# Kernel optimization log

Measured on AMD Instinct MI355X. Metric: run time of the kernel, lower is better.

The kernel has to match this reference:

```python
import jax, jax.numpy as jnp
import numpy as np
import math

L, D, H = 4, 256, 8
HD = D // H
B, SQ, SK = 2, 1024, 1024
FF = 3 * D
EPS = 1e-5


def setup_inputs() -> dict:
    key = jax.random.key(0)
    ks = jax.random.split(key, 16)
    s = 0.02
    w = lambda k, shape: jax.random.normal(k, shape, jnp.float32) * s
    return {
        "pose": jax.random.normal(ks[0], (B, SQ, D), jnp.float32),
        "vel": jax.random.normal(ks[1], (B, SK, D), jnp.float32),
        "img": jax.random.normal(ks[2], (B, SK, D), jnp.float32),
        "Wq": w(ks[3], (L, D, D)), "bq": jnp.zeros((L, D), jnp.float32),
        "Wk": w(ks[4], (L, D, D)), "bk": jnp.zeros((L, D), jnp.float32),
        "Wv": w(ks[5], (L, D, D)), "bv": jnp.zeros((L, D), jnp.float32),
        "Wo": w(ks[6], (L, D, D)), "bo": jnp.zeros((L, D), jnp.float32),
        "an_g": jnp.ones((L, D), jnp.float32), "an_b": jnp.zeros((L, D), jnp.float32),
        "W1": w(ks[7], (L, D, FF)), "b1": jnp.zeros((L, FF), jnp.float32),
        "W2": w(ks[8], (L, FF, D)), "b2": jnp.zeros((L, D), jnp.float32),
        "fn_g": jnp.ones((L, D), jnp.float32), "fn_b": jnp.zeros((L, D), jnp.float32),
        "n_g": jnp.ones((L, D), jnp.float32), "n_b": jnp.zeros((L, D), jnp.float32),
    }


def entmax15(x):
    # exact alpha=1.5 entmax along the last axis (Peters & Martins 2019)
    x = x * 0.5
    x = x - jnp.max(x, axis=-1, keepdims=True)
    z = -jnp.sort(-x, axis=-1)  # descending
    k = jnp.arange(1, z.shape[-1] + 1, dtype=x.dtype)
    mean = jnp.cumsum(z, axis=-1) / k
    mean_sq = jnp.cumsum(z * z, axis=-1) / k
    ss = k * (mean_sq - mean * mean)
    delta = jnp.clip((1.0 - ss) / k, 0.0)
    tau = mean - jnp.sqrt(delta)
    support = jnp.sum(tau <= z, axis=-1, keepdims=True)  # support size >= 1
    tau_star = jnp.take_along_axis(tau, support - 1, axis=-1)
    p = jnp.clip(x - tau_star, 0.0)
    return p * p


def layer_norm(x, g, b):
    m = jnp.mean(x, axis=-1, keepdims=True)
    v = jnp.mean((x - m) ** 2, axis=-1, keepdims=True)
    return (x - m) * jax.lax.rsqrt(v + EPS) * g + b


def mish(x):
    return x * jnp.tanh(jax.nn.softplus(x))


def reference(pose, vel, img, Wq, bq, Wk, bk, Wv, bv, Wo, bo, an_g, an_b,
              W1, b1, W2, b2, fn_g, fn_b, n_g, n_b):
    def mha(q_in, kv, i):
        bs, sq, _ = q_in.shape
        sk = kv.shape[1]
        q = (q_in @ Wq[i] + bq[i]).reshape(bs, sq, H, HD)
        k = (kv @ Wk[i] + bk[i]).reshape(bs, sk, H, HD)
        v = (kv @ Wv[i] + bv[i]).reshape(bs, sk, H, HD)
        scores = jnp.einsum('bqhd,bkhd->bhqk', q, k) / math.sqrt(HD)
        attn = entmax15(scores)
        out = jnp.einsum('bhqk,bkhd->bqhd', attn, v).reshape(bs, sq, D)
        return out @ Wo[i] + bo[i]

    def cross_layer(x1, x2, i):
        y = layer_norm(mha(x1, x2, i), an_g[i], an_b[i])
        x1 = x1 + y
        y = layer_norm(x1, fn_g[i], fn_b[i])
        h = mish(y @ W1[i] + b1[i]) @ W2[i] + b2[i]
        return x1 + h

    def stack(x, kv):
        for i in range(L):  # small fixed layer loop (shared weights across both paths)
            mem = x
            x = cross_layer(x, kv, i)
            x = layer_norm(x, n_g[i], n_b[i])
            x = x + mem
        return x

    img_out = stack(pose, img)
    pose_out = stack(pose, vel)
    return (pose_out, img_out)
```

## Files before the change

### kernel.cpp

```cpp
#include <hip/hip_runtime.h>
#include <math.h>

#define NL   4
#define DIM  256
#define NH   8
#define HDIM 32
#define SQL  1024
#define SKL  1024
#define FFD  768
#define CB   4
#define ROWS (CB * SQL)

typedef __attribute__((ext_vector_type(8))) short bf16x8;
typedef __attribute__((ext_vector_type(4))) short bf16x4;
typedef __attribute__((ext_vector_type(4))) float f32x4;
typedef __attribute__((ext_vector_type(2))) float f32x2;


__device__ __forceinline__ short f2bf(float f) {
    union { float f; unsigned u; } v; v.f = f;
    unsigned u = v.u + 0x7fffu + ((v.u >> 16) & 1u);
    return (short)(u >> 16);
}

__device__ __forceinline__ float fast_mish(float x) {
    float u = __expf(fminf(x, 20.0f));
    float a = __builtin_fmaf(u, u, 2.0f * u);
    return x * a * __builtin_amdgcn_rcpf(a + 2.0f);
}

__device__ __forceinline__ f32x2 lo2(f32x4 v) { return __builtin_shufflevector(v, v, 0, 1); }
__device__ __forceinline__ f32x2 hi2(f32x4 v) { return __builtin_shufflevector(v, v, 2, 3); }


__global__ __launch_bounds__(256) void init_kernel(
        const float* __restrict__ pose, const float* __restrict__ vel,
        const float* __restrict__ img, float* __restrict__ X,
        short* __restrict__ Xb, short* __restrict__ KVb) {
    int idx = blockIdx.x * 256 + threadIdx.x;
    if (idx >= CB * SQL * DIM) return;
    int c = idx / (SQL * DIM);
    int rem = idx - c * (SQL * DIM);
    int b = c & 1;
    float pv = pose[b * SQL * DIM + rem];
    X[idx]  = pv;
    Xb[idx] = f2bf(pv);
    const float* kv = (c < 2) ? vel : img;
    KVb[idx] = f2bf(kv[b * SQL * DIM + rem]);
}


__global__ __launch_bounds__(256) void transpose_all(
        const float* __restrict__ Wq, const float* __restrict__ Wk,
        const float* __restrict__ Wv, const float* __restrict__ Wo,
        const float* __restrict__ W1, const float* __restrict__ W2,
        short* __restrict__ Wqt, short* __restrict__ Wkt,
        short* __restrict__ Wvt, short* __restrict__ Wot,
        short* __restrict__ W1t, short* __restrict__ W2t) {
    __shared__ float tile[64][65];
    int z = blockIdx.x;
    const float* src; short* dst; int K, N, tx, ty;
    if (z < 256) {
        int m = z >> 6, lyr = (z >> 4) & 3, r = z & 15;
        src = ((m == 0) ? Wq : (m == 1) ? Wk : (m == 2) ? Wv : Wo) + (size_t)lyr * DIM * DIM;
        dst = ((m == 0) ? Wqt : (m == 1) ? Wkt : (m == 2) ? Wvt : Wot) + (size_t)lyr * DIM * DIM;
        K = DIM; N = DIM; tx = r & 3; ty = r >> 2;
    } else if (z < 448) {
        int idx = z - 256, lyr = idx / 48, r = idx % 48;
        src = W1 + (size_t)lyr * DIM * FFD; dst = W1t + (size_t)lyr * DIM * FFD;
        K = DIM; N = FFD; tx = r % 12; ty = r / 12;
    } else {
        int idx = z - 448, lyr = idx / 48, r = idx % 48;
        src = W2 + (size_t)lyr * FFD * DIM; dst = W2t + (size_t)lyr * FFD * DIM;
        K = FFD; N = DIM; tx = r % 4; ty = r / 4;
    }
    int t = threadIdx.x;
    int n0 = tx * 64, k0 = ty * 64;
#pragma unroll
    for (int i = 0; i < 16; i++) {
        int idx = t + i * 256;
        int r = idx >> 6, c = idx & 63;
        tile[r][c] = src[(size_t)(k0 + r) * N + n0 + c];
    }
    __syncthreads();
#pragma unroll
    for (int i = 0; i < 16; i++) {
        int idx = t + i * 256;
        int r = idx >> 6, c = idx & 63;
        dst[(size_t)(n0 + r) * K + k0 + c] = f2bf(tile[c][r]);
    }
}


__global__ __launch_bounds__(256) void qkv_gemm(
        const short* __restrict__ Xb, const short* __restrict__ KVb,
        const short* __restrict__ Wqt, const short* __restrict__ Wkt,
        const short* __restrict__ Wvt,
        const float* __restrict__ bq, const float* __restrict__ bk,
        const float* __restrict__ bv,
        short* __restrict__ Qb, short* __restrict__ Kb, short* __restrict__ Vt,
        float qscale) {
    int z = blockIdx.z;
    const short* A    = (z == 0) ? Xb : KVb;
    const short* Wt   = (z == 0) ? Wqt : (z == 1) ? Wkt : Wvt;
    const float* bias = (z == 0) ? bq : (z == 1) ? bk : bv;
    float scale = (z == 0) ? qscale : 1.0f;

    int t = threadIdx.x, l = t & 63, w = t >> 6;
    int lq = l & 15, lg = l >> 4;
    int bm = blockIdx.y * 64, bn = blockIdx.x * 64;

    const short* ap = A + (size_t)(bm + w * 16 + lq) * DIM + lg * 8;
    const short* wp = Wt + (size_t)(bn + lq) * DIM + lg * 8;

    f32x4 acc[4];
#pragma unroll
    for (int nt = 0; nt < 4; nt++) acc[nt] = (f32x4){0.f, 0.f, 0.f, 0.f};
#pragma unroll
    for (int k0 = 0; k0 < DIM; k0 += 32) {
        bf16x8 af = *(const bf16x8*)(ap + k0);
#pragma unroll
        for (int nt = 0; nt < 4; nt++) {
            bf16x8 bfr = *(const bf16x8*)(wp + (size_t)nt * 16 * DIM + k0);
            acc[nt] = __builtin_amdgcn_mfma_f32_16x16x32_bf16(af, bfr, acc[nt], 0, 0, 0);
        }
    }

    int ms = bm + w * 16 + lg * 4;
#pragma unroll
    for (int nt = 0; nt < 4; nt++) {
        int col = bn + nt * 16 + lq;
        float bv_ = bias[col];
        float v[4];
#pragma unroll
        for (int j = 0; j < 4; j++) v[j] = acc[nt][j] + bv_;
        if (z < 2) {
            short* out = (z == 0) ? Qb : Kb;
#pragma unroll
            for (int j = 0; j < 4; j++) out[(size_t)(ms + j) * DIM + col] = f2bf(v[j] * scale);
        } else {
            int cc = ms >> 10, kl = ms & 1023;
            bf16x4 pk;
#pragma unroll
            for (int j = 0; j < 4; j++) pk[j] = f2bf(v[j]);
            *(bf16x4*)(Vt + ((size_t)(cc * DIM + col)) * SKL + kl) = pk;
        }
    }
}


__global__ __launch_bounds__(512) void fused_tail(
        const short* __restrict__ T1b, const short* __restrict__ Wot,
        const float* __restrict__ bo, const float* __restrict__ Xres,
        const float* __restrict__ ag, const float* __restrict__ ab,
        const float* __restrict__ fg, const float* __restrict__ fb,
        const short* __restrict__ W1t, const float* __restrict__ b1,
        const short* __restrict__ W2t, const float* __restrict__ b2,
        const float* __restrict__ g_, const float* __restrict__ b_,
        float* __restrict__ outf, short* __restrict__ outb) {
    __shared__ float gbuf[16][264];
    __shared__ __align__(16) short y_lds[16][280];
    __shared__ __align__(16) short g1[16][792];
    float (*xbuf)[264] = (float(*)[264])g1;

    int t = threadIdx.x, l = t & 63, w = t >> 6;
    int lq = l & 15, lg = l >> 4;
    int bm = blockIdx.x * 16;

    {
        const short* ap = T1b + (size_t)(bm + lq) * DIM + lg * 8;
        const short* wp = Wot + (size_t)(w * 32 + lq) * DIM + lg * 8;
        f32x4 acc[2];
        acc[0] = (f32x4){0.f, 0.f, 0.f, 0.f};
        acc[1] = (f32x4){0.f, 0.f, 0.f, 0.f};
#pragma unroll
        for (int k0 = 0; k0 < DIM; k0 += 32) {
            bf16x8 af = *(const bf16x8*)(ap + k0);
#pragma unroll
            for (int nt = 0; nt < 2; nt++) {
                bf16x8 bfr = *(const bf16x8*)(wp + (size_t)nt * 16 * DIM + k0);
                acc[nt] = __builtin_amdgcn_mfma_f32_16x16x32_bf16(af, bfr, acc[nt], 0, 0, 0);
            }
        }
#pragma unroll
        for (int nt = 0; nt < 2; nt++) {
            int col = w * 32 + nt * 16 + lq;
            float bv_ = bo[col];
#pragma unroll
            for (int j = 0; j < 4; j++) gbuf[lg * 4 + j][col] = acc[nt][j] + bv_;
        }
    }
    __syncthreads();

    {
        int g = t >> 5, u = t & 31;
        int row = bm + g;
        float s = 0.f, s2 = 0.f;
#pragma unroll
        for (int i = 0; i < 8; i++) {
            float v = gbuf[g][u + 32 * i];
            s += v; s2 += v * v;
        }
#pragma unroll
        for (int off = 1; off < 32; off <<= 1) { s += __shfl_xor(s, off); s2 += __shfl_xor(s2, off); }
        float m = s * (1.f / DIM);
        float rstd = rsqrtf(s2 * (1.f / DIM) - m * m + 1e-5f);

        float x1v[8];
        float sb = 0.f, sb2 = 0.f;
#pragma unroll
        for (int i = 0; i < 8; i++) {
            int col = u + 32 * i;
            float x1 = Xres[(size_t)row * DIM + col] + (gbuf[g][col] - m) * rstd * ag[col] + ab[col];
            x1v[i] = x1; sb += x1; sb2 += x1 * x1;
        }
#pragma unroll
        for (int off = 1; off < 32; off <<= 1) { sb += __shfl_xor(sb, off); sb2 += __shfl_xor(sb2, off); }
        float m2 = sb * (1.f / DIM);
        float rstd2 = rsqrtf(sb2 * (1.f / DIM) - m2 * m2 + 1e-5f);
#pragma unroll
        for (int i = 0; i < 8; i++) {
            int col = u + 32 * i;
            gbuf[g][col]  = x1v[i];
            y_lds[g][col] = f2bf((x1v[i] - m2) * rstd2 * fg[col] + fb[col]);
        }
    }
    __syncthreads();

    {
        const short* wp = W1t + (size_t)(w * 96 + lq) * DIM + lg * 8;
        f32x4 acc[6];
#pragma unroll
        for (int nt = 0; nt < 6; nt++) acc[nt] = (f32x4){0.f, 0.f, 0.f, 0.f};
#pragma unroll
        for (int k0 = 0; k0 < DIM; k0 += 32) {
            bf16x8 af = *(const bf16x8*)(&y_lds[lq][k0 + lg * 8]);
#pragma unroll
            for (int nt = 0; nt < 6; nt++) {
                bf16x8 bfr = *(const bf16x8*)(wp + (size_t)nt * 16 * DIM + k0);
                acc[nt] = __builtin_amdgcn_mfma_f32_16x16x32_bf16(af, bfr, acc[nt], 0, 0, 0);
            }
        }
#pragma unroll
        for (int nt = 0; nt < 6; nt++) {
            int col = w * 96 + nt * 16 + lq;
            float bv_ = b1[col];
#pragma unroll
            for (int j = 0; j < 4; j++)
                g1[lg * 4 + j][col] = f2bf(fast_mish(acc[nt][j] + bv_));
        }
    }
    __syncthreads();

    f32x4 acc2[2];
    acc2[0] = (f32x4){0.f, 0.f, 0.f, 0.f};
    acc2[1] = (f32x4){0.f, 0.f, 0.f, 0.f};
    {
        const short* wp2 = W2t + (size_t)(w * 32 + lq) * FFD + lg * 8;
#pragma unroll 6
        for (int ks = 0; ks < 24; ks++) {
            bf16x8 af = *(const bf16x8*)(&g1[lq][ks * 32 + lg * 8]);
#pragma unroll
            for (int nt = 0; nt < 2; nt++) {
                bf16x8 bfr = *(const bf16x8*)(wp2 + (size_t)nt * 16 * FFD + ks * 32);
                acc2[nt] = __builtin_amdgcn_mfma_f32_16x16x32_bf16(af, bfr, acc2[nt], 0, 0, 0);
            }
        }
    }
    __syncthreads();
#pragma unroll
    for (int nt = 0; nt < 2; nt++) {
        int col = w * 32 + nt * 16 + lq;
        float bv_ = b2[col];
#pragma unroll
        for (int j = 0; j < 4; j++)
            xbuf[lg * 4 + j][col] = acc2[nt][j] + bv_ + gbuf[lg * 4 + j][col];
    }
    __syncthreads();

    {
        int g = t >> 5, u = t & 31;
        int row = bm + g;
        float s = 0.f, s2 = 0.f;
#pragma unroll
        for (int i = 0; i < 8; i++) {
            float v = xbuf[g][u + 32 * i];
            s += v; s2 += v * v;
        }
#pragma unroll
        for (int off = 1; off < 32; off <<= 1) { s += __shfl_xor(s, off); s2 += __shfl_xor(s2, off); }
        float m = s * (1.f / DIM);
        float rstd = rsqrtf(s2 * (1.f / DIM) - m * m + 1e-5f);
#pragma unroll
        for (int i = 0; i < 8; i++) {
            int col = u + 32 * i;
            float o = Xres[(size_t)row * DIM + col] + (xbuf[g][col] - m) * rstd * g_[col] + b_[col];
            outf[(size_t)row * DIM + col] = o;
            if (outb) outb[(size_t)row * DIM + col] = f2bf(o);
        }
    }
}


__global__ __launch_bounds__(256, 4) void attn_mfma(
        const short* __restrict__ Q, const short* __restrict__ K,
        const short* __restrict__ Vt, short* __restrict__ O) {
    int h = blockIdx.y, c = blockIdx.z;
    int qbase = blockIdx.x * 16;
    int t = threadIdx.x, l = t & 63, w = t >> 6;
    int lq = l & 15, lg = l >> 4;

    __shared__ __align__(16) short p_lds[4][1024];
    __shared__ float obuf[4][512];
    __shared__ float redf[2][3][4][16];

    bf16x8 qfrag = *(const bf16x8*)(Q + ((size_t)(c * SQL + qbase + lq)) * DIM + h * HDIM + lg * 8);

    const int kw = w * 256;
    f32x4 acc[16];
#pragma unroll
    for (int kt = 0; kt < 16; kt++) {
        bf16x8 kf = *(const bf16x8*)(K + ((size_t)(c * SKL + kw + kt * 16 + lq)) * DIM + h * HDIM + lg * 8);
        f32x4 z = {0.f, 0.f, 0.f, 0.f};
        acc[kt] = __builtin_amdgcn_mfma_f32_16x16x32_bf16(kf, qfrag, z, 0, 0, 0);
    }

    const f32x2 z2  = {0.f, 0.f};
    const f32x2 big = {1e30f, 1e30f};
    const f32x2 one = {1.f, 1.f};

    f32x2 mm = lo2(acc[0]);
#pragma unroll
    for (int kt = 0; kt < 16; kt++) {
        mm = __builtin_elementwise_max(mm, lo2(acc[kt]));
        mm = __builtin_elementwise_max(mm, hi2(acc[kt]));
    }
    float m = fmaxf(mm.x, mm.y);
    m = fmaxf(m, __shfl_xor(m, 16));
    m = fmaxf(m, __shfl_xor(m, 32));
    if (l < 16) redf[1][0][w][l] = m;
    __syncthreads();
    m = fmaxf(fmaxf(redf[1][0][0][lq], redf[1][0][1][lq]),
              fmaxf(redf[1][0][2][lq], redf[1][0][3][lq]));

    float tau = m - 1.0f;
    int r = 0;
    for (;;) {
        f32x2 vt = {tau, tau};
        f32x2 S1 = z2, S2 = z2, NN = z2;
#pragma unroll
        for (int kt = 0; kt < 16; kt++) {
            f32x2 y0 = __builtin_elementwise_max(lo2(acc[kt]) - vt, z2);
            f32x2 y1 = __builtin_elementwise_max(hi2(acc[kt]) - vt, z2);
            S1 += y0; S1 += y1;
            S2 += y0 * y0; S2 += y1 * y1;
            NN += __builtin_elementwise_min(y0 * big, one);
            NN += __builtin_elementwise_min(y1 * big, one);
        }
        float sy = S1.x + S1.y, sy2 = S2.x + S2.y, nn = NN.x + NN.y;
        sy  += __shfl_xor(sy, 16);  sy  += __shfl_xor(sy, 32);
        sy2 += __shfl_xor(sy2, 16); sy2 += __shfl_xor(sy2, 32);
        nn  += __shfl_xor(nn, 16);  nn  += __shfl_xor(nn, 32);
        int b = r & 1;
        if (l < 16) { redf[b][0][w][l] = nn; redf[b][1][w][l] = sy; redf[b][2][w][l] = sy2; }
        __syncthreads();
        nn  = redf[b][0][0][lq] + redf[b][0][1][lq] + redf[b][0][2][lq] + redf[b][0][3][lq];
        sy  = redf[b][1][0][lq] + redf[b][1][1][lq] + redf[b][1][2][lq] + redf[b][1][3][lq];
        sy2 = redf[b][2][0][lq] + redf[b][2][1][lq] + redf[b][2][2][lq] + redf[b][2][3][lq];
        float disc = fmaxf(sy * sy - nn * (sy2 - 1.0f), 0.f);
        float delta = (sy - sqrtf(disc)) / nn;
        tau = fminf(tau + delta, m - 0.03125f);
        r++;
        if (r >= 6 || __all(delta < 1e-6f)) break;
    }

    f32x4 o0 = {0.f, 0.f, 0.f, 0.f}, o1 = {0.f, 0.f, 0.f, 0.f};
    const short* vbase0 = Vt + ((size_t)(c * DIM + h * HDIM + lq)) * SKL;
    const short* vbase1 = vbase0 + (size_t)16 * SKL;
    {
        f32x2 vt = {tau, tau};
        int swz = (lq & 7) << 4;
#pragma unroll
        for (int c2 = 0; c2 < 4; c2++) {
#pragma unroll
            for (int k4 = 0; k4 < 4; k4++) {
                int kt = c2 * 4 + k4;
                f32x2 y0 = __builtin_elementwise_max(lo2(acc[kt]) - vt, z2);
                f32x2 y1 = __builtin_elementwise_max(hi2(acc[kt]) - vt, z2);
                f32x2 p0 = y0 * y0, p1 = y1 * y1;
                unsigned u01, u23;
                asm("v_cvt_pk_bf16_f32 %0, %1, %2" : "=v"(u01) : "v"(p0.x), "v"(p0.y));
                asm("v_cvt_pk_bf16_f32 %0, %1, %2" : "=v"(u23) : "v"(p1.x), "v"(p1.y));
                int klocal = k4 * 16 + lg * 4;
                int byte = lq * 128 + ((klocal * 2) ^ swz);
                *(uint2*)((char*)p_lds[w] + byte) = make_uint2(u01, u23);
            }
#pragma unroll
            for (int k2 = 0; k2 < 2; k2++) {
                int klocal0 = k2 * 32 + lg * 8;
                int byte = lq * 128 + ((klocal0 * 2) ^ swz);
                bf16x8 pa = *(const bf16x8*)((const char*)p_lds[w] + byte);
                int k0 = kw + c2 * 64 + klocal0;
                bf16x8 vb0 = *(const bf16x8*)(vbase0 + k0);
                bf16x8 vb1 = *(const bf16x8*)(vbase1 + k0);
                o0 = __builtin_amdgcn_mfma_f32_16x16x32_bf16(pa, vb0, o0, 0, 0, 0);
                o1 = __builtin_amdgcn_mfma_f32_16x16x32_bf16(pa, vb1, o1, 0, 0, 0);
            }
        }
    }

#pragma unroll
    for (int j = 0; j < 4; j++) {
        obuf[w][(lg * 4 + j) * 32 + lq]      = o0[j];
        obuf[w][(lg * 4 + j) * 32 + 16 + lq] = o1[j];
    }
    __syncthreads();
#pragma unroll
    for (int rep = 0; rep < 2; rep++) {
        int e = t + rep * 256;
        int q = e >> 5, d = e & 31;
        float s = obuf[0][e] + obuf[1][e] + obuf[2][e] + obuf[3][e];
        O[((size_t)(c * SQL + qbase + q)) * DIM + h * HDIM + d] = f2bf(s);
    }
}


extern "C" void kernel_launch(void* const* d_in, const int* in_sizes, int n_in,
                              void* d_out, int out_size, void* d_ws, size_t ws_size,
                              hipStream_t stream) {
    const float* pose = (const float*)d_in[0];
    const float* vel  = (const float*)d_in[1];
    const float* img  = (const float*)d_in[2];
    const float* Wq   = (const float*)d_in[3];
    const float* bq   = (const float*)d_in[4];
    const float* Wk   = (const float*)d_in[5];
    const float* bk   = (const float*)d_in[6];
    const float* Wv   = (const float*)d_in[7];
    const float* bv   = (const float*)d_in[8];
    const float* Wo   = (const float*)d_in[9];
    const float* bo   = (const float*)d_in[10];
    const float* an_g = (const float*)d_in[11];
    const float* an_b = (const float*)d_in[12];
    const float* W1   = (const float*)d_in[13];
    const float* b1   = (const float*)d_in[14];
    const float* W2   = (const float*)d_in[15];
    const float* b2   = (const float*)d_in[16];
    const float* fn_g = (const float*)d_in[17];
    const float* fn_b = (const float*)d_in[18];
    const float* n_g  = (const float*)d_in[19];
    const float* n_b  = (const float*)d_in[20];

    const size_t SZ = (size_t)ROWS * DIM;
    float* X    = (float*)d_ws;
    short* Xb   = (short*)(X + SZ);
    short* KVb  = Xb + SZ;
    short* T1b  = KVb + SZ;
    short* Qb   = T1b + SZ;
    short* Kb   = Qb + SZ;
    short* Vt   = Kb + SZ;
    short* Wqt  = Vt + SZ;
    short* Wkt  = Wqt + (size_t)NL * DIM * DIM;
    short* Wvt  = Wkt + (size_t)NL * DIM * DIM;
    short* Wot  = Wvt + (size_t)NL * DIM * DIM;
    short* W1t  = Wot + (size_t)NL * DIM * DIM;
    short* W2t  = W1t + (size_t)NL * DIM * FFD;

    {
        int total = CB * SQL * DIM;
        init_kernel<<<(total + 255) / 256, 256, 0, stream>>>(pose, vel, img, X, Xb, KVb);
    }
    transpose_all<<<640, 256, 0, stream>>>(Wq, Wk, Wv, Wo, W1, W2,
                                           Wqt, Wkt, Wvt, Wot, W1t, W2t);

    const float qscale = 0.08838834764831845f;

    for (int i = 0; i < NL; i++) {
        const short* Wqt_i = Wqt + (size_t)i * DIM * DIM;
        const short* Wkt_i = Wkt + (size_t)i * DIM * DIM;
        const short* Wvt_i = Wvt + (size_t)i * DIM * DIM;
        const short* Wot_i = Wot + (size_t)i * DIM * DIM;
        const short* W1t_i = W1t + (size_t)i * DIM * FFD;
        const short* W2t_i = W2t + (size_t)i * DIM * FFD;

        qkv_gemm<<<dim3(DIM / 64, ROWS / 64, 3), 256, 0, stream>>>(
            Xb, KVb, Wqt_i, Wkt_i, Wvt_i,
            bq + i * DIM, bk + i * DIM, bv + i * DIM, Qb, Kb, Vt, qscale);

        attn_mfma<<<dim3(SQL / 16, NH, CB), 256, 0, stream>>>(Qb, Kb, Vt, T1b);

        float* outp  = (i == NL - 1) ? (float*)d_out : X;
        short* outbp = (i == NL - 1) ? nullptr : Xb;
        fused_tail<<<ROWS / 16, 512, 0, stream>>>(
            T1b, Wot_i, bo + i * DIM, X,
            an_g + i * DIM, an_b + i * DIM, fn_g + i * DIM, fn_b + i * DIM,
            W1t_i, b1 + i * FFD, W2t_i, b2 + i * DIM,
            n_g + i * DIM, n_b + i * DIM, outp, outbp);
    }

    (void)in_sizes; (void)n_in; (void)out_size; (void)ws_size;
}
```

Before: 388.5 us.

## Split attention keys across eight waves and remap blocks for XCD locality

The attention kernel now runs 512 threads per block with eight waves, each handling 128 keys instead of 256. That halves per-wave accumulator registers and raises occupancy through a launch bound of six blocks. The grid is flattened and remapped so each XCD processes a contiguous set of (head, batch) pairs, aiming for better L2 reuse of K and V. Cross-wave reductions now use vectorized LDS reads and packed bf16 output stores; the cost is more shared memory per block and more cross-wave synchronization per entmax iteration.

```diff
diff --git a/kernel.cpp b/kernel.cpp
--- a/kernel.cpp
+++ b/kernel.cpp
@@ -302,24 +302,27 @@
 }
 
 
-__global__ __launch_bounds__(256, 4) void attn_mfma(
+__global__ __launch_bounds__(512, 6) void attn_mfma(
         const short* __restrict__ Q, const short* __restrict__ K,
         const short* __restrict__ Vt, short* __restrict__ O) {
-    int h = blockIdx.y, c = blockIdx.z;
-    int qbase = blockIdx.x * 16;
+    int id = blockIdx.x;
+    int xcd = id & 7, rest = id >> 3;
+    int hc = xcd * 4 + (rest >> 6);
+    int c = hc & 3, h = hc >> 2;
+    int qbase = (rest & 63) * 16;
     int t = threadIdx.x, l = t & 63, w = t >> 6;
     int lq = l & 15, lg = l >> 4;
 
-    __shared__ __align__(16) short p_lds[4][1024];
-    __shared__ float obuf[4][512];
-    __shared__ float redf[2][3][4][16];
+    __shared__ __align__(16) short p_lds[8][1024];
+    __shared__ float obuf[8][512];
+    __shared__ __align__(16) float sred[2][3][16][8];
 
     bf16x8 qfrag = *(const bf16x8*)(Q + ((size_t)(c * SQL + qbase + lq)) * DIM + h * HDIM + lg * 8);
 
-    const int kw = w * 256;
-    f32x4 acc[16];
-#pragma unroll
-    for (int kt = 0; kt < 16; kt++) {
+    const int kw = w * 128;
+    f32x4 acc[8];
+#pragma unroll
+    for (int kt = 0; kt < 8; kt++) {
         bf16x8 kf = *(const bf16x8*)(K + ((size_t)(c * SKL + kw + kt * 16 + lq)) * DIM + h * HDIM + lg * 8);
         f32x4 z = {0.f, 0.f, 0.f, 0.f};
         acc[kt] = __builtin_amdgcn_mfma_f32_16x16x32_bf16(kf, qfrag, z, 0, 0, 0);
@@ -331,17 +334,21 @@
 
     f32x2 mm = lo2(acc[0]);
 #pragma unroll
-    for (int kt = 0; kt < 16; kt++) {
+    for (int kt = 0; kt < 8; kt++) {
         mm = __builtin_elementwise_max(mm, lo2(acc[kt]));
         mm = __builtin_elementwise_max(mm, hi2(acc[kt]));
     }
     float m = fmaxf(mm.x, mm.y);
     m = fmaxf(m, __shfl_xor(m, 16));
     m = fmaxf(m, __shfl_xor(m, 32));
-    if (l < 16) redf[1][0][w][l] = m;
-    __syncthreads();
-    m = fmaxf(fmaxf(redf[1][0][0][lq], redf[1][0][1][lq]),
-              fmaxf(redf[1][0][2][lq], redf[1][0][3][lq]));
+    if (l < 16) sred[1][0][l][w] = m;
+    __syncthreads();
+    {
+        f32x4 a = *(const f32x4*)sred[1][0][lq];
+        f32x4 b = *(const f32x4*)(sred[1][0][lq] + 4);
+        f32x4 mx = __builtin_elementwise_max(a, b);
+        m = fmaxf(fmaxf(mx[0], mx[1]), fmaxf(mx[2], mx[3]));
+    }
 
     float tau = m - 1.0f;
     int r = 0;
@@ -349,7 +356,7 @@
         f32x2 vt = {tau, tau};
         f32x2 S1 = z2, S2 = z2, NN = z2;
 #pragma unroll
-        for (int kt = 0; kt < 16; kt++) {
+        for (int kt = 0; kt < 8; kt++) {
             f32x2 y0 = __builtin_elementwise_max(lo2(acc[kt]) - vt, z2);
             f32x2 y1 = __builtin_elementwise_max(hi2(acc[kt]) - vt, z2);
             S1 += y0; S1 += y1;
@@ -362,11 +369,20 @@
         sy2 += __shfl_xor(sy2, 16); sy2 += __shfl_xor(sy2, 32);
         nn  += __shfl_xor(nn, 16);  nn  += __shfl_xor(nn, 32);
         int b = r & 1;
-        if (l < 16) { redf[b][0][w][l] = nn; redf[b][1][w][l] = sy; redf[b][2][w][l] = sy2; }
+        if (l < 16) { sred[b][0][l][w] = nn; sred[b][1][l][w] = sy; sred[b][2][l][w] = sy2; }
         __syncthreads();
-        nn  = redf[b][0][0][lq] + redf[b][0][1][lq] + redf[b][0][2][lq] + redf[b][0][3][lq];
-        sy  = redf[b][1][0][lq] + redf[b][1][1][lq] + redf[b][1][2][lq] + redf[b][1][3][lq];
-        sy2 = redf[b][2][0][lq] + redf[b][2][1][lq] + redf[b][2][2][lq] + redf[b][2][3][lq];
+        {
+            f32x4 n0 = *(const f32x4*)sred[b][0][lq];
+            f32x4 n1 = *(const f32x4*)(sred[b][0][lq] + 4);
+            f32x4 s0 = *(const f32x4*)sred[b][1][lq];
+            f32x4 s1 = *(const f32x4*)(sred[b][1][lq] + 4);
+            f32x4 q0 = *(const f32x4*)sred[b][2][lq];
+            f32x4 q1 = *(const f32x4*)(sred[b][2][lq] + 4);
+            f32x4 ns = n0 + n1, ss = s0 + s1, qs = q0 + q1;
+            nn  = ns[0] + ns[1] + ns[2] + ns[3];
+            sy  = ss[0] + ss[1] + ss[2] + ss[3];
+            sy2 = qs[0] + qs[1] + qs[2] + qs[3];
+        }
         float disc = fmaxf(sy * sy - nn * (sy2 - 1.0f), 0.f);
         float delta = (sy - sqrtf(disc)) / nn;
         tau = fminf(tau + delta, m - 0.03125f);
@@ -381,7 +397,7 @@
         f32x2 vt = {tau, tau};
         int swz = (lq & 7) << 4;
 #pragma unroll
-        for (int c2 = 0; c2 < 4; c2++) {
+        for (int c2 = 0; c2 < 2; c2++) {
 #pragma unroll
             for (int k4 = 0; k4 < 4; k4++) {
                 int kt = c2 * 4 + k4;
@@ -391,16 +407,14 @@
                 unsigned u01, u23;
                 asm("v_cvt_pk_bf16_f32 %0, %1, %2" : "=v"(u01) : "v"(p0.x), "v"(p0.y));
                 asm("v_cvt_pk_bf16_f32 %0, %1, %2" : "=v"(u23) : "v"(p1.x), "v"(p1.y));
-                int klocal = k4 * 16 + lg * 4;
-                int byte = lq * 128 + ((klocal * 2) ^ swz);
+                int byte = lq * 128 + ((k4 * 32 + lg * 8) ^ swz);
                 *(uint2*)((char*)p_lds[w] + byte) = make_uint2(u01, u23);
             }
 #pragma unroll
             for (int k2 = 0; k2 < 2; k2++) {
-                int klocal0 = k2 * 32 + lg * 8;
-                int byte = lq * 128 + ((klocal0 * 2) ^ swz);
+                int byte = lq * 128 + ((k2 * 64 + lg * 16) ^ swz);
                 bf16x8 pa = *(const bf16x8*)((const char*)p_lds[w] + byte);
-                int k0 = kw + c2 * 64 + klocal0;
+                int k0 = kw + c2 * 64 + k2 * 32 + lg * 8;
                 bf16x8 vb0 = *(const bf16x8*)(vbase0 + k0);
                 bf16x8 vb1 = *(const bf16x8*)(vbase1 + k0);
                 o0 = __builtin_amdgcn_mfma_f32_16x16x32_bf16(pa, vb0, o0, 0, 0, 0);
@@ -415,12 +429,15 @@
         obuf[w][(lg * 4 + j) * 32 + 16 + lq] = o1[j];
     }
     __syncthreads();
-#pragma unroll
-    for (int rep = 0; rep < 2; rep++) {
-        int e = t + rep * 256;
-        int q = e >> 5, d = e & 31;
-        float s = obuf[0][e] + obuf[1][e] + obuf[2][e] + obuf[3][e];
-        O[((size_t)(c * SQL + qbase + q)) * DIM + h * HDIM + d] = f2bf(s);
+    if (t < 256) {
+        int e0 = t * 2;
+        int q = e0 >> 5, d = e0 & 31;
+        f32x2 s = *(const f32x2*)&obuf[0][e0];
+#pragma unroll
+        for (int ww = 1; ww < 8; ww++) s += *(const f32x2*)&obuf[ww][e0];
+        unsigned uo;
+        asm("v_cvt_pk_bf16_f32 %0, %1, %2" : "=v"(uo) : "v"(s.x), "v"(s.y));
+        *(unsigned*)(O + ((size_t)(c * SQL + qbase + q)) * DIM + h * HDIM + d) = uo;
     }
 }
 
@@ -486,7 +503,7 @@
             Xb, KVb, Wqt_i, Wkt_i, Wvt_i,
             bq + i * DIM, bk + i * DIM, bv + i * DIM, Qb, Kb, Vt, qscale);
 
-        attn_mfma<<<dim3(SQL / 16, NH, CB), 256, 0, stream>>>(Qb, Kb, Vt, T1b);
+        attn_mfma<<<2048, 512, 0, stream>>>(Qb, Kb, Vt, T1b);
 
         float* outp  = (i == NL - 1) ? (float*)d_out : X;
         short* outbp = (i == NL - 1) ? nullptr : Xb;
```

After: 408.6 us. 5.2% more time.
